# Performance work log

Measured on AMD Instinct MI355X. Metric: run time of the kernel, lower is better.

Reference implementation:

```python
import jax, jax.numpy as jnp
import numpy as np

EPS = 1e-12  # matches torch F.normalize default eps


def _l2_normalize(x, axis=-1):
    norm = jnp.sqrt(jnp.sum(x * x, axis=axis, keepdims=True))
    return x / jnp.maximum(norm, EPS)


def setup_inputs() -> dict:
    key = jax.random.key(0)
    k1, k2 = jax.random.split(key)
    B, D, P = 8192, 512, 32768
    z_context = jax.random.normal(k1, (B, D), dtype=jnp.float32)
    prototypes = jax.random.normal(k2, (P, D), dtype=jnp.float32) * 0.02
    return {"z_context": z_context, "prototypes": prototypes, "topk": 3}


def reference(z_context, prototypes, topk):
    # Cosine similarity: normalize queries and prototype bank, then GEMM.
    z_norm = _l2_normalize(z_context, axis=-1)          # [B, D]
    p_norm = _l2_normalize(prototypes, axis=-1)         # [P, D]
    sim = jnp.einsum('bd,pd->bp', z_norm, p_norm)       # [B, P]
    k = min(topk, prototypes.shape[0])
    topk_val, topk_idx = jax.lax.top_k(sim, k)          # [B, k] each
    return sim, topk_idx, topk_val
```

## Files before the change

### kernel.cpp

```cpp
#include <hip/hip_runtime.h>
#include <float.h>
#include <stdint.h>

#define D_DIM 512

typedef __attribute__((ext_vector_type(8))) short bf16x8;
typedef __attribute__((ext_vector_type(4))) float f32x4;

#define GLD_LDS16(g, l)                                              \
    __builtin_amdgcn_global_load_lds(                                \
        (const __attribute__((address_space(1))) void*)(g),          \
        (__attribute__((address_space(3))) void*)(l), 16, 0, 0)

__device__ __forceinline__ uint32_t pk_bf16(float a, float b) {
    uint32_t ua = __builtin_bit_cast(uint32_t, a) + 0x8000u;
    uint32_t ub = __builtin_bit_cast(uint32_t, b) + 0x8000u;
    return (ua >> 16) | (ub & 0xFFFF0000u);
}

__global__ __launch_bounds__(256) void convert_norm_kernel(
        const float* __restrict__ X, unsigned short* __restrict__ Xb,
        float* __restrict__ r, int R) {
    int row = blockIdx.x * 4 + (threadIdx.x >> 6);
    if (row >= R) return;
    int lane = threadIdx.x & 63;
    const float* x = X + (size_t)row * D_DIM + lane * 8;
    float4 f0 = *(const float4*)(x);
    float4 f1 = *(const float4*)(x + 4);
    float s = f0.x*f0.x + f0.y*f0.y + f0.z*f0.z + f0.w*f0.w
            + f1.x*f1.x + f1.y*f1.y + f1.z*f1.z + f1.w*f1.w;
#pragma unroll
    for (int off = 32; off; off >>= 1) s += __shfl_xor(s, off);
    float rv = 1.0f / fmaxf(sqrtf(s), 1e-12f);
    if (lane == 0) r[row] = rv;
    uint4 w;
    w.x = pk_bf16(f0.x * rv, f0.y * rv);
    w.y = pk_bf16(f0.z * rv, f0.w * rv);
    w.z = pk_bf16(f1.x * rv, f1.y * rv);
    w.w = pk_bf16(f1.z * rv, f1.w * rv);
    *(uint4*)(Xb + (size_t)row * D_DIM + lane * 8) = w;
}

template <bool FUSE>
__global__ __launch_bounds__(256, 4) void gemm_lds_bf16(
        const unsigned short* __restrict__ Zb,
        const unsigned short* __restrict__ Pb,
        float* __restrict__ sim, uint2* __restrict__ part, int Pn) {
    __shared__ __align__(16) unsigned char SH[32768];
    uint4* S = (uint4*)SH;

    int bi = blockIdx.x;
    int mb, nb;
    if (gridDim.x == 16384) {
        int xcd = bi & 7;
        int r = bi >> 3;
        mb = xcd * 8 + (r & 7);
        nb = r >> 3;
    } else {
        nb = bi % (Pn / 128);
        mb = bi / (Pn / 128);
    }
    const int bm = mb * 128, bn = nb * 128;

    const int tid = threadIdx.x;
    const int lane = tid & 63;
    const int wid = tid >> 6;
    const int wr = wid >> 1, wc = wid & 1;
    const int ln15 = lane & 15, hi = lane >> 4;

    const unsigned short* gA[2];
    const unsigned short* gB[2];
    int ldsIdx[2];
#pragma unroll
    for (int q = 0; q < 2; ++q) {
        int flat = q * 256 + tid;
        int row = flat >> 2;
        int c = flat & 3;
        int cg = c ^ (row & 3);
        gA[q] = Zb + (size_t)(bm + row) * D_DIM + cg * 8;
        gB[q] = Pb + (size_t)(bn + row) * D_DIM + cg * 8;
        ldsIdx[q] = flat;
    }

    f32x4 acc[4][4] = {};

#pragma unroll
    for (int q = 0; q < 2; ++q) {
        GLD_LDS16(gA[q], &S[ldsIdx[q]]);
        GLD_LDS16(gB[q], &S[512 + ldsIdx[q]]);
        gA[q] += 32;
        gB[q] += 32;
    }

    int cur = 0;
#pragma unroll 1
    for (int s8 = 0; s8 < 16; ++s8) {
        const int nxt = cur ^ 1;
        if (s8 < 15) {
#pragma unroll
            for (int q = 0; q < 2; ++q) {
                GLD_LDS16(gA[q], &S[nxt * 1024 + ldsIdx[q]]);
                GLD_LDS16(gB[q], &S[nxt * 1024 + 512 + ldsIdx[q]]);
                gA[q] += 32;
                gB[q] += 32;
            }
            asm volatile("s_waitcnt vmcnt(4)" ::: "memory");
        } else {
            asm volatile("s_waitcnt vmcnt(0)" ::: "memory");
        }
        __builtin_amdgcn_s_barrier();
        __builtin_amdgcn_sched_barrier(0);

        const int sb = cur * 1024;
        __builtin_amdgcn_s_setprio(1);
        bf16x8 av[4], bv[4];
#pragma unroll
        for (int t = 0; t < 4; ++t) {
            int arow = wr * 64 + t * 16 + ln15;
            av[t] = __builtin_bit_cast(bf16x8,
                    S[sb + arow * 4 + (hi ^ (arow & 3))]);
            int brow = wc * 64 + t * 16 + ln15;
            bv[t] = __builtin_bit_cast(bf16x8,
                    S[sb + 512 + brow * 4 + (hi ^ (brow & 3))]);
        }
#pragma unroll
        for (int i = 0; i < 4; ++i)
#pragma unroll
            for (int j = 0; j < 4; ++j)
                acc[i][j] = __builtin_amdgcn_mfma_f32_16x16x32_bf16(
                    av[i], bv[j], acc[i][j], 0, 0, 0);
        __builtin_amdgcn_s_setprio(0);
        __builtin_amdgcn_sched_barrier(0);
        __builtin_amdgcn_s_barrier();
        cur = nxt;
    }

#pragma unroll
    for (int i = 0; i < 4; ++i) {
#pragma unroll
        for (int rr = 0; rr < 4; ++rr) {
            int row = bm + wr * 64 + i * 16 + hi * 4 + rr;
#pragma unroll
            for (int j = 0; j < 4; ++j) {
                int col = bn + wc * 64 + j * 16 + ln15;
                sim[(size_t)row * Pn + col] = acc[i][j][rr];
            }
        }
    }

    if constexpr (FUSE) {
        float* T = (float*)SH;
        uint2* M = (uint2*)(SH + 17408);
        const int NB = Pn >> 7;
        const int r = tid & 63;
        const int q = tid >> 6;
#pragma unroll 1
        for (int hf = 0; hf < 2; ++hf) {
            float rv[4]; int ri[4];
#pragma unroll
            for (int k = 0; k < 4; ++k) { rv[k] = -FLT_MAX; ri[k] = 0x7FFFFFFF; }
#pragma unroll 1
            for (int ch = 0; ch < 2; ++ch) {
                __syncthreads();
                if (wr == hf && wc == ch) {
#pragma unroll
                    for (int i = 0; i < 4; ++i)
#pragma unroll
                        for (int j = 0; j < 4; ++j)
                            *(f32x4*)&T[(j * 16 + ln15) * 68 + i * 16 + hi * 4]
                                = acc[i][j];
                }
                __syncthreads();
                float tv[4]; int ti[4];
#pragma unroll
                for (int k = 0; k < 4; ++k) { tv[k] = -FLT_MAX; ti[k] = 0x7FFFFFFF; }
#pragma unroll
                for (int c4 = 0; c4 < 16; c4 += 4) {
                    float e0 = T[(q * 16 + c4 + 0) * 68 + r];
                    float e1 = T[(q * 16 + c4 + 1) * 68 + r];
                    float e2 = T[(q * 16 + c4 + 2) * 68 + r];
                    float e3 = T[(q * 16 + c4 + 3) * 68 + r];
                    float mg = fmaxf(fmaxf(e0, e1), fmaxf(e2, e3));
                    if (mg > tv[3]) {
                        float ee[4] = {e0, e1, e2, e3};
#pragma unroll
                        for (int e = 0; e < 4; ++e) {
                            float val = ee[e];
                            if (val > tv[3]) {
                                int p = 3;
#pragma unroll
                                for (int j2 = 2; j2 >= 0; --j2)
                                    if (val > tv[j2]) { tv[j2+1] = tv[j2]; ti[j2+1] = ti[j2]; p = j2; }
                                tv[p] = val; ti[p] = bn + ch * 64 + q * 16 + c4 + e;
                            }
                        }
                    }
                }
#pragma unroll
                for (int k = 0; k < 4; ++k)
                    M[q * 256 + k * 64 + r] =
                        make_uint2(__builtin_bit_cast(uint32_t, tv[k]), (uint32_t)ti[k]);
                __syncthreads();
                if (tid < 64) {
#pragma unroll
                    for (int qq = 0; qq < 4; ++qq)
#pragma unroll
                        for (int k = 0; k < 4; ++k) {
                            uint2 u = M[qq * 256 + k * 64 + tid];
                            float val = __builtin_bit_cast(float, u.x);
                            if (val > rv[3]) {
                                int p = 3;
#pragma unroll
                                for (int j2 = 2; j2 >= 0; --j2)
                                    if (val > rv[j2]) { rv[j2+1] = rv[j2]; ri[j2+1] = ri[j2]; p = j2; }
                                rv[p] = val; ri[p] = (int)u.y;
                            }
                        }
                }
            }
            if (tid < 64) {
                size_t o = ((size_t)(bm + hf * 64 + tid) * NB + nb) * 4;
#pragma unroll
                for (int k = 0; k < 4; ++k)
                    part[o + k] =
                        make_uint2(__builtin_bit_cast(uint32_t, rv[k]), (uint32_t)ri[k]);
            }
        }
    }
}

__global__ __launch_bounds__(256) void topk_reduce(const uint2* __restrict__ part,
        const float* __restrict__ Z, const float* __restrict__ Pm,
        const float* __restrict__ rz, const float* __restrict__ rp,
        float* __restrict__ oidx, float* __restrict__ oval, int Pn) {
    int row = blockIdx.x * 4 + (threadIdx.x >> 6);
    int lane = threadIdx.x & 63;
    const int NB = Pn >> 7;
    const uint2* pr = part + (size_t)row * NB * 4;

    float v[8]; int ix[8];
#pragma unroll
    for (int j = 0; j < 8; ++j) { v[j] = -FLT_MAX; ix[j] = -1; }

    const int total = NB * 4;
    for (int c = lane; c < total; c += 64) {
        uint2 u = pr[c];
        float val = __builtin_bit_cast(float, u.x);
        if (val > v[7]) {
            int idx = (int)u.y;
            int pos = 7;
#pragma unroll
            for (int j = 6; j >= 0; --j) {
                if (val > v[j]) { v[j+1] = v[j]; ix[j+1] = ix[j]; pos = j; }
            }
            v[pos] = val; ix[pos] = idx;
        }
    }

    int cand[8];
#pragma unroll
    for (int k = 0; k < 8; ++k) {
        float bv = v[0]; int bi2 = ix[0];
#pragma unroll
        for (int off = 32; off; off >>= 1) {
            float ov = __shfl_xor(bv, off);
            int oi = __shfl_xor(bi2, off);
            if (ov > bv || (ov == bv && oi >= 0 && (unsigned)oi < (unsigned)bi2)) {
                bv = ov; bi2 = oi;
            }
        }
        cand[k] = bi2;
        if (bi2 == ix[0]) {
#pragma unroll
            for (int j = 0; j < 7; ++j) { v[j] = v[j+1]; ix[j] = ix[j+1]; }
            v[7] = -FLT_MAX; ix[7] = -1;
        }
    }

    float zv[8];
    const float* zrow = Z + (size_t)row * D_DIM + lane * 8;
#pragma unroll
    for (int j = 0; j < 8; ++j) zv[j] = zrow[j];
    float rzv = rz[row];

    float ex[8];
#pragma unroll
    for (int c = 0; c < 8; ++c) {
        int idx = cand[c];
        const float* prow = Pm + (size_t)idx * D_DIM + lane * 8;
        float s = 0.f;
#pragma unroll
        for (int j = 0; j < 8; ++j) s += zv[j] * prow[j];
#pragma unroll
        for (int off = 32; off; off >>= 1) s += __shfl_xor(s, off);
        ex[c] = s * rzv * rp[idx];
    }

    bool used[8] = {};
#pragma unroll
    for (int k = 0; k < 3; ++k) {
        float bv = -FLT_MAX; int bi2 = Pn; int bc = 0;
#pragma unroll
        for (int c = 0; c < 8; ++c) {
            if (!used[c] && (ex[c] > bv || (ex[c] == bv && cand[c] < bi2))) {
                bv = ex[c]; bi2 = cand[c]; bc = c;
            }
        }
        used[bc] = true;
        if (lane == 0) {
            oidx[(size_t)row * 3 + k] = (float)bi2;
            oval[(size_t)row * 3 + k] = bv;
        }
    }
}

__global__ __launch_bounds__(256) void rnorm_kernel(const float* __restrict__ X,
                                                    float* __restrict__ r, int R) {
    int row = blockIdx.x * 4 + (threadIdx.x >> 6);
    if (row >= R) return;
    int lane = threadIdx.x & 63;
    const float* x = X + (size_t)row * D_DIM;
    float s = 0.f;
#pragma unroll
    for (int t = 0; t < 2; ++t) {
        float4 v = *(const float4*)(x + (t * 64 + lane) * 4);
        s += v.x * v.x + v.y * v.y + v.z * v.z + v.w * v.w;
    }
#pragma unroll
    for (int off = 32; off; off >>= 1) s += __shfl_xor(s, off);
    if (lane == 0) r[row] = 1.0f / fmaxf(sqrtf(s), 1e-12f);
}

__global__ __launch_bounds__(256, 2) void gemm_bf16_sim(const float* __restrict__ Z,
        const float* __restrict__ Pm, const float* __restrict__ rz,
        const float* __restrict__ rp, float* __restrict__ sim, int Pn) {
    __shared__ uint4 As16[1024];
    __shared__ uint4 Bs16[1024];
    int bi = blockIdx.x;
    int mb, nb;
    if (gridDim.x == 16384) {
        int xcd = bi & 7;
        int r = bi >> 3;
        mb = xcd * 8 + (r & 7);
        nb = r >> 3;
    } else {
        nb = bi % (Pn / 128);
        mb = bi / (Pn / 128);
    }
    const int bm = mb * 128, bn = nb * 128;
    const int tid = threadIdx.x;
    const int srow = tid >> 1;
    const int half = tid & 1;
    const float* aP = Z  + (size_t)(bm + srow) * D_DIM + half * 32;
    const float* bP = Pm + (size_t)(bn + srow) * D_DIM + half * 32;
    const int lane = tid & 63;
    const int wid = tid >> 6;
    const int wr = wid >> 1, wc = wid & 1;
    const int ln15 = lane & 15, hi = lane >> 4;
    f32x4 acc[4][4] = {};
    float4 f[8], g[8];
#pragma unroll
    for (int q = 0; q < 8; ++q) {
        f[q] = *(const float4*)(aP + q * 4);
        g[q] = *(const float4*)(bP + q * 4);
    }
#pragma unroll 1
    for (int s = 0; s < 8; ++s) {
#pragma unroll
        for (int q8 = 0; q8 < 4; ++q8) {
            uint4 wa, wb;
            wa.x = pk_bf16(f[2*q8].x,   f[2*q8].y);
            wa.y = pk_bf16(f[2*q8].z,   f[2*q8].w);
            wa.z = pk_bf16(f[2*q8+1].x, f[2*q8+1].y);
            wa.w = pk_bf16(f[2*q8+1].z, f[2*q8+1].w);
            wb.x = pk_bf16(g[2*q8].x,   g[2*q8].y);
            wb.y = pk_bf16(g[2*q8].z,   g[2*q8].w);
            wb.z = pk_bf16(g[2*q8+1].x, g[2*q8+1].y);
            wb.w = pk_bf16(g[2*q8+1].z, g[2*q8+1].w);
            int colByte = half * 64 + q8 * 16;
            int idx = srow * 8 + ((colByte ^ ((srow & 7) << 4)) >> 4);
            As16[idx] = wa;
            Bs16[idx] = wb;
        }
        __syncthreads();
        if (s < 7) {
            int k0 = (s + 1) * 64;
#pragma unroll
            for (int q = 0; q < 8; ++q) {
                f[q] = *(const float4*)(aP + k0 + q * 4);
                g[q] = *(const float4*)(bP + k0 + q * 4);
            }
        }
#pragma unroll
        for (int kk = 0; kk < 2; ++kk) {
            bf16x8 av[4], bv[4];
            const int cb = kk * 64 + hi * 16;
#pragma unroll
            for (int t = 0; t < 4; ++t) {
                int arow = wr * 64 + t * 16 + ln15;
                av[t] = __builtin_bit_cast(bf16x8,
                        As16[arow * 8 + ((cb ^ ((arow & 7) << 4)) >> 4)]);
                int brow = wc * 64 + t * 16 + ln15;
                bv[t] = __builtin_bit_cast(bf16x8,
                        Bs16[brow * 8 + ((cb ^ ((brow & 7) << 4)) >> 4)]);
            }
#pragma unroll
            for (int i = 0; i < 4; ++i)
#pragma unroll
                for (int j = 0; j < 4; ++j)
                    acc[i][j] = __builtin_amdgcn_mfma_f32_16x16x32_bf16(
                        av[i], bv[j], acc[i][j], 0, 0, 0);
        }
        __syncthreads();
    }
    float rpv[4];
#pragma unroll
    for (int j = 0; j < 4; ++j) rpv[j] = rp[bn + wc * 64 + j * 16 + ln15];
#pragma unroll
    for (int i = 0; i < 4; ++i) {
#pragma unroll
        for (int rr = 0; rr < 4; ++rr) {
            int row = bm + wr * 64 + i * 16 + hi * 4 + rr;
            float rzv = rz[row];
#pragma unroll
            for (int j = 0; j < 4; ++j) {
                int col = bn + wc * 64 + j * 16 + ln15;
                sim[(size_t)row * Pn + col] = acc[i][j][rr] * rzv * rpv[j];
            }
        }
    }
}

__global__ __launch_bounds__(256) void topk_refine(const float* __restrict__ sim,
        const float* __restrict__ Z, const float* __restrict__ Pm,
        const float* __restrict__ rz, const float* __restrict__ rp,
        float* __restrict__ oidx, float* __restrict__ oval, int Pn) {
    int row = blockIdx.x * 4 + (threadIdx.x >> 6);
    int lane = threadIdx.x & 63;
    const float* rptr = sim + (size_t)row * Pn;

    float v[8]; int ix[8];
#pragma unroll
    for (int j = 0; j < 8; ++j) { v[j] = -FLT_MAX; ix[j] = -1; }

    const int iters = Pn >> 8;
    for (int t = 0; t < iters; ++t) {
        int base = t * 256 + lane * 4;
        float4 q = *(const float4*)(rptr + base);
        float vals[4] = {q.x, q.y, q.z, q.w};
#pragma unroll
        for (int e = 0; e < 4; ++e) {
            float val = vals[e];
            if (val > v[7]) {
                int idx = base + e;
                int pos = 7;
#pragma unroll
                for (int j = 6; j >= 0; --j) {
                    if (val > v[j]) { v[j+1] = v[j]; ix[j+1] = ix[j]; pos = j; }
                }
                v[pos] = val; ix[pos] = idx;
            }
        }
    }

    int cand[8];
#pragma unroll
    for (int k = 0; k < 8; ++k) {
        float bv = v[0]; int bi2 = ix[0];
#pragma unroll
        for (int off = 32; off; off >>= 1) {
            float ov = __shfl_xor(bv, off);
            int oi = __shfl_xor(bi2, off);
            if (ov > bv || (ov == bv && oi >= 0 && (unsigned)oi < (unsigned)bi2)) {
                bv = ov; bi2 = oi;
            }
        }
        cand[k] = bi2;
        if (bi2 == ix[0]) {
#pragma unroll
            for (int j = 0; j < 7; ++j) { v[j] = v[j+1]; ix[j] = ix[j+1]; }
            v[7] = -FLT_MAX; ix[7] = -1;
        }
    }

    float zv[8];
    const float* zrow = Z + (size_t)row * D_DIM + lane * 8;
#pragma unroll
    for (int j = 0; j < 8; ++j) zv[j] = zrow[j];
    float rzv = rz[row];

    float ex[8];
#pragma unroll
    for (int c = 0; c < 8; ++c) {
        int idx = cand[c];
        const float* prow = Pm + (size_t)idx * D_DIM + lane * 8;
        float s = 0.f;
#pragma unroll
        for (int j = 0; j < 8; ++j) s += zv[j] * prow[j];
#pragma unroll
        for (int off = 32; off; off >>= 1) s += __shfl_xor(s, off);
        ex[c] = s * rzv * rp[idx];
    }

    bool used[8] = {};
#pragma unroll
    for (int k = 0; k < 3; ++k) {
        float bv = -FLT_MAX; int bi2 = Pn; int bc = 0;
#pragma unroll
        for (int c = 0; c < 8; ++c) {
            if (!used[c] && (ex[c] > bv || (ex[c] == bv && cand[c] < bi2))) {
                bv = ex[c]; bi2 = cand[c]; bc = c;
            }
        }
        used[bc] = true;
        if (lane == 0) {
            oidx[(size_t)row * 3 + k] = (float)bi2;
            oval[(size_t)row * 3 + k] = bv;
        }
    }
}

extern "C" void kernel_launch(void* const* d_in, const int* in_sizes, int n_in,
                              void* d_out, int out_size, void* d_ws, size_t ws_size,
                              hipStream_t stream) {
    const float* Z  = (const float*)d_in[0];
    const float* Pm = (const float*)d_in[1];
    const int B  = in_sizes[0] / D_DIM;
    const int Pn = in_sizes[1] / D_DIM;

    float* sim  = (float*)d_out;
    float* oidx = sim + (size_t)B * Pn;
    float* oval = oidx + (size_t)B * 3;

    float* rz = (float*)d_ws;
    float* rp = rz + B;
    unsigned short* Zb = (unsigned short*)(rp + Pn);
    unsigned short* Pb = Zb + (size_t)B * D_DIM;
    uint2* part = (uint2*)(Pb + (size_t)Pn * D_DIM);

    const size_t NB = (size_t)Pn / 128;
    const size_t need_bf16  = (size_t)(B + Pn) * 4 + (size_t)(B + Pn) * D_DIM * 2;
    const size_t need_fused = need_bf16 + (size_t)B * NB * 4 * sizeof(uint2);

    dim3 grid((B / 128) * (Pn / 128));

    if (ws_size >= need_fused) {
        convert_norm_kernel<<<B / 4, 256, 0, stream>>>(Z, Zb, rz, B);
        convert_norm_kernel<<<Pn / 4, 256, 0, stream>>>(Pm, Pb, rp, Pn);
        gemm_lds_bf16<true><<<grid, 256, 0, stream>>>(Zb, Pb, sim, part, Pn);
        topk_reduce<<<B / 4, 256, 0, stream>>>(part, Z, Pm, rz, rp, oidx, oval, Pn);
    } else if (ws_size >= need_bf16) {
        convert_norm_kernel<<<B / 4, 256, 0, stream>>>(Z, Zb, rz, B);
        convert_norm_kernel<<<Pn / 4, 256, 0, stream>>>(Pm, Pb, rp, Pn);
        gemm_lds_bf16<false><<<grid, 256, 0, stream>>>(Zb, Pb, sim, nullptr, Pn);
        topk_refine<<<B / 4, 256, 0, stream>>>(sim, Z, Pm, rz, rp, oidx, oval, Pn);
    } else {
        rnorm_kernel<<<B / 4, 256, 0, stream>>>(Z, rz, B);
        rnorm_kernel<<<Pn / 4, 256, 0, stream>>>(Pm, rp, Pn);
        gemm_bf16_sim<<<grid, 256, 0, stream>>>(Z, Pm, rz, rp, sim, Pn);
        topk_refine<<<B / 4, 256, 0, stream>>>(sim, Z, Pm, rz, rp, oidx, oval, Pn);
    }
}
```

Before: 695.6 us.

## Add 256x256-tile fused GEMM with coalesced sim stores and per-tile top-k

Adds a new 512-thread GEMM kernel that uses 256x256 output tiles with a 64-wide K step, double-buffered direct global-to-LDS loads and 128 KB of dynamic shared memory. It fuses the top-k partial selection and writes sim through an LDS transpose, so each thread stores full float4 rows. The larger tile halves redundant operand reads and halves the number of partial top-k entries the reduce kernel has to scan. In exchange it holds more accumulator registers per thread and needs a large LDS allocation, which may limit occupancy. The insertion sort is also rewritten as a macro.

```diff
diff --git a/kernel.cpp b/kernel.cpp
--- a/kernel.cpp
+++ b/kernel.cpp
@@ -17,6 +17,15 @@
     uint32_t ub = __builtin_bit_cast(uint32_t, b) + 0x8000u;
     return (ua >> 16) | (ub & 0xFFFF0000u);
 }
+
+#define INS4(val, idx, tv, ti)                                        \
+    if ((val) > tv[3]) {                                              \
+        int p_ = 3;                                                   \
+        if ((val) > tv[2]) { tv[3] = tv[2]; ti[3] = ti[2]; p_ = 2; }  \
+        if ((val) > tv[1]) { tv[2] = tv[1]; ti[2] = ti[1]; p_ = 1; }  \
+        if ((val) > tv[0]) { tv[1] = tv[0]; ti[1] = ti[0]; p_ = 0; }  \
+        tv[p_] = (val); ti[p_] = (idx);                               \
+    }
 
 __global__ __launch_bounds__(256) void convert_norm_kernel(
         const float* __restrict__ X, unsigned short* __restrict__ Xb,
@@ -41,13 +50,274 @@
     *(uint4*)(Xb + (size_t)row * D_DIM + lane * 8) = w;
 }
 
+__global__ __launch_bounds__(512, 2) void gemm256_fused(
+        const unsigned short* __restrict__ Zb,
+        const unsigned short* __restrict__ Pb,
+        float* __restrict__ sim, uint2* __restrict__ part, int Pn) {
+    extern __shared__ __align__(16) unsigned char SH[];
+    uint4* S = (uint4*)SH;
+
+    int bi = blockIdx.x;
+    int mb, nb;
+    if (gridDim.x == 4096) {
+        int xcd = bi & 7, r = bi >> 3;
+        mb = xcd * 4 + (r & 3);
+        nb = r >> 2;
+    } else {
+        int nt = Pn >> 8;
+        nb = bi % nt; mb = bi / nt;
+    }
+    const int bm = mb << 8, bn = nb << 8;
+
+    const int tid = threadIdx.x;
+    const int lane = tid & 63;
+    const int wid = tid >> 6;
+    const int wr = wid >> 2;
+    const int wc = wid & 3;
+    const int ln15 = lane & 15, hi = lane >> 4;
+
+    const int fl0 = tid, fl1 = 512 + tid;
+    const int rl0 = fl0 >> 3, rl1 = fl1 >> 3;
+    const int cg0 = (fl0 & 7) ^ (rl0 & 7);
+    const int cg1 = (fl1 & 7) ^ (rl1 & 7);
+
+    const unsigned short* pA0q0 = Zb + (size_t)(bm + rl0) * D_DIM + cg0 * 8;
+    const unsigned short* pA0q1 = Zb + (size_t)(bm + rl1) * D_DIM + cg1 * 8;
+    const unsigned short* pA1q0 = Zb + (size_t)(bm + 128 + rl0) * D_DIM + cg0 * 8;
+    const unsigned short* pA1q1 = Zb + (size_t)(bm + 128 + rl1) * D_DIM + cg1 * 8;
+    const unsigned short* pB0q0 = Pb + (size_t)(bn + rl0) * D_DIM + cg0 * 8;
+    const unsigned short* pB0q1 = Pb + (size_t)(bn + rl1) * D_DIM + cg1 * 8;
+    const unsigned short* pB1q0 = Pb + (size_t)(bn + 128 + rl0) * D_DIM + cg0 * 8;
+    const unsigned short* pB1q1 = Pb + (size_t)(bn + 128 + rl1) * D_DIM + cg1 * 8;
+
+    const int dA0q0 = fl0,        dA0q1 = fl1;
+    const int dA1q0 = 1024 + fl0, dA1q1 = 1024 + fl1;
+    const int dB0q0 = 4096 + fl0, dB0q1 = 4096 + fl1;
+    const int dB1q0 = 5120 + fl0, dB1q1 = 5120 + fl1;
+
+    const int sw0 = hi ^ (ln15 & 7);
+    const int sw1 = (4 + hi) ^ (ln15 & 7);
+    int aOff[8], bOff[4];
+#pragma unroll
+    for (int m = 0; m < 8; ++m) aOff[m] = (wr * 128 + m * 16 + ln15) * 8;
+#pragma unroll
+    for (int n = 0; n < 4; ++n) bOff[n] = 4096 + (wc * 64 + n * 16 + ln15) * 8;
+
+    f32x4 acc[8][4] = {};
+
+    GLD_LDS16(pA0q0, &S[dA0q0]); GLD_LDS16(pA0q1, &S[dA0q1]);
+    GLD_LDS16(pA1q0, &S[dA1q0]); GLD_LDS16(pA1q1, &S[dA1q1]);
+    GLD_LDS16(pB0q0, &S[dB0q0]); GLD_LDS16(pB0q1, &S[dB0q1]);
+    GLD_LDS16(pB1q0, &S[dB1q0]); GLD_LDS16(pB1q1, &S[dB1q1]);
+    pA0q0 += 64; pA0q1 += 64; pA1q0 += 64; pA1q1 += 64;
+    pB0q0 += 64; pB0q1 += 64; pB1q0 += 64; pB1q1 += 64;
+    asm volatile("s_waitcnt vmcnt(0)" ::: "memory");
+    __builtin_amdgcn_s_barrier();
+
+#pragma unroll 1
+    for (int t = 0; t < 8; ++t) {
+        const int db = (t & 1) * 2048;
+        const int dn = ((t + 1) & 1) * 2048;
+        const bool more = (t < 7);
+#pragma unroll
+        for (int p = 0; p < 4; ++p) {
+            const int mh = p >> 1, nh = p & 1;
+            bf16x8 av[4][2], bv[2][2];
+#pragma unroll
+            for (int mi = 0; mi < 4; ++mi) {
+                av[mi][0] = __builtin_bit_cast(bf16x8, S[db + aOff[mh * 4 + mi] + sw0]);
+                av[mi][1] = __builtin_bit_cast(bf16x8, S[db + aOff[mh * 4 + mi] + sw1]);
+            }
+#pragma unroll
+            for (int ni = 0; ni < 2; ++ni) {
+                bv[ni][0] = __builtin_bit_cast(bf16x8, S[db + bOff[nh * 2 + ni] + sw0]);
+                bv[ni][1] = __builtin_bit_cast(bf16x8, S[db + bOff[nh * 2 + ni] + sw1]);
+            }
+            if (p == 0 && more) {
+                GLD_LDS16(pB0q0, &S[dn + dB0q0]); GLD_LDS16(pB0q1, &S[dn + dB0q1]);
+                GLD_LDS16(pA0q0, &S[dn + dA0q0]); GLD_LDS16(pA0q1, &S[dn + dA0q1]);
+                pB0q0 += 64; pB0q1 += 64; pA0q0 += 64; pA0q1 += 64;
+            }
+            if (p == 1 && more) {
+                GLD_LDS16(pB1q0, &S[dn + dB1q0]); GLD_LDS16(pB1q1, &S[dn + dB1q1]);
+                GLD_LDS16(pA1q0, &S[dn + dA1q0]); GLD_LDS16(pA1q1, &S[dn + dA1q1]);
+                pB1q0 += 64; pB1q1 += 64; pA1q0 += 64; pA1q1 += 64;
+            }
+            __builtin_amdgcn_s_barrier();
+            asm volatile("s_waitcnt lgkmcnt(0)" ::: "memory");
+            __builtin_amdgcn_sched_barrier(0);
+            __builtin_amdgcn_s_setprio(1);
+#pragma unroll
+            for (int kk = 0; kk < 2; ++kk)
+#pragma unroll
+                for (int mi = 0; mi < 4; ++mi)
+#pragma unroll
+                    for (int ni = 0; ni < 2; ++ni)
+                        acc[mh * 4 + mi][nh * 2 + ni] =
+                            __builtin_amdgcn_mfma_f32_16x16x32_bf16(
+                                av[mi][kk], bv[ni][kk],
+                                acc[mh * 4 + mi][nh * 2 + ni], 0, 0, 0);
+            __builtin_amdgcn_s_setprio(0);
+            __builtin_amdgcn_sched_barrier(0);
+            if (p < 3) __builtin_amdgcn_s_barrier();
+        }
+        if (more) asm volatile("s_waitcnt vmcnt(0)" ::: "memory");
+        __builtin_amdgcn_s_barrier();
+    }
+
+    float* T = (float*)SH;
+    const int NB = Pn >> 8;
+    const int r = tid >> 2;
+    const int g = tid & 3;
+#pragma unroll 1
+    for (int hf = 0; hf < 2; ++hf) {
+        float tv[4]; int ti[4];
+#pragma unroll
+        for (int k = 0; k < 4; ++k) { tv[k] = -FLT_MAX; ti[k] = 0x7FFFFFFF; }
+#pragma unroll 1
+        for (int ch = 0; ch < 2; ++ch) {
+            __syncthreads();
+            if (wr == hf && (wc >> 1) == ch) {
+#pragma unroll
+                for (int m = 0; m < 8; ++m)
+#pragma unroll
+                    for (int n = 0; n < 4; ++n)
+                        *(f32x4*)&T[((wc & 1) * 64 + n * 16 + ln15) * 132
+                                    + m * 16 + hi * 4] = acc[m][n];
+            }
+            __syncthreads();
+            const int colBase = bn + ch * 128;
+            float* srow = sim + (size_t)(bm + hf * 128 + r) * Pn + colBase;
+#pragma unroll
+            for (int j = 0; j < 8; ++j) {
+                const int c0 = j * 16 + g * 4;
+                float e0 = T[(c0 + 0) * 132 + r];
+                float e1 = T[(c0 + 1) * 132 + r];
+                float e2 = T[(c0 + 2) * 132 + r];
+                float e3 = T[(c0 + 3) * 132 + r];
+                float4 o; o.x = e0; o.y = e1; o.z = e2; o.w = e3;
+                *(float4*)&srow[c0] = o;
+                float mg = fmaxf(fmaxf(e0, e1), fmaxf(e2, e3));
+                if (mg > tv[3]) {
+                    INS4(e0, colBase + c0 + 0, tv, ti);
+                    INS4(e1, colBase + c0 + 1, tv, ti);
+                    INS4(e2, colBase + c0 + 2, tv, ti);
+                    INS4(e3, colBase + c0 + 3, tv, ti);
+                }
+            }
+        }
+#pragma unroll
+        for (int st = 1; st <= 2; st <<= 1) {
+            float ov0 = __shfl_xor(tv[0], st), ov1 = __shfl_xor(tv[1], st);
+            float ov2 = __shfl_xor(tv[2], st), ov3 = __shfl_xor(tv[3], st);
+            int oi0 = __shfl_xor(ti[0], st), oi1 = __shfl_xor(ti[1], st);
+            int oi2 = __shfl_xor(ti[2], st), oi3 = __shfl_xor(ti[3], st);
+            INS4(ov0, oi0, tv, ti);
+            INS4(ov1, oi1, tv, ti);
+            INS4(ov2, oi2, tv, ti);
+            INS4(ov3, oi3, tv, ti);
+        }
+        if (g == 0) {
+            size_t o = ((size_t)(bm + hf * 128 + r) * NB + nb) * 4;
+#pragma unroll
+            for (int k = 0; k < 4; ++k)
+                part[o + k] =
+                    make_uint2(__builtin_bit_cast(uint32_t, tv[k]), (uint32_t)ti[k]);
+        }
+    }
+}
+
+__global__ __launch_bounds__(256) void topk_reduce(const uint2* __restrict__ part,
+        const float* __restrict__ Z, const float* __restrict__ Pm,
+        const float* __restrict__ rz, const float* __restrict__ rp,
+        float* __restrict__ oidx, float* __restrict__ oval, int Pn, int NB) {
+    int row = blockIdx.x * 4 + (threadIdx.x >> 6);
+    int lane = threadIdx.x & 63;
+    const uint2* pr = part + (size_t)row * NB * 4;
+
+    float v[8]; int ix[8];
+#pragma unroll
+    for (int j = 0; j < 8; ++j) { v[j] = -FLT_MAX; ix[j] = -1; }
+
+    const int total = NB * 4;
+    for (int c = lane; c < total; c += 64) {
+        uint2 u = pr[c];
+        float val = __builtin_bit_cast(float, u.x);
+        if (val > v[7]) {
+            int idx = (int)u.y;
+            int pos = 7;
+#pragma unroll
+            for (int j = 6; j >= 0; --j) {
+                if (val > v[j]) { v[j+1] = v[j]; ix[j+1] = ix[j]; pos = j; }
+            }
+            v[pos] = val; ix[pos] = idx;
+        }
+    }
+
+    int cand[8];
+#pragma unroll
+    for (int k = 0; k < 8; ++k) {
+        float bv = v[0]; int bi2 = ix[0];
+#pragma unroll
+        for (int off = 32; off; off >>= 1) {
+            float ov = __shfl_xor(bv, off);
+            int oi = __shfl_xor(bi2, off);
+            if (ov > bv || (ov == bv && oi >= 0 && (unsigned)oi < (unsigned)bi2)) {
+                bv = ov; bi2 = oi;
+            }
+        }
+        cand[k] = bi2;
+        if (bi2 == ix[0]) {
+#pragma unroll
+            for (int j = 0; j < 7; ++j) { v[j] = v[j+1]; ix[j] = ix[j+1]; }
+            v[7] = -FLT_MAX; ix[7] = -1;
+        }
+    }
+
+    float zv[8];
+    const float* zrow = Z + (size_t)row * D_DIM + lane * 8;
+#pragma unroll
+    for (int j = 0; j < 8; ++j) zv[j] = zrow[j];
+    float rzv = rz[row];
+
+    float ex[8];
+#pragma unroll
+    for (int c = 0; c < 8; ++c) {
+        int idx = cand[c];
+        const float* prow = Pm + (size_t)idx * D_DIM + lane * 8;
+        float s = 0.f;
+#pragma unroll
+        for (int j = 0; j < 8; ++j) s += zv[j] * prow[j];
+#pragma unroll
+        for (int off = 32; off; off >>= 1) s += __shfl_xor(s, off);
+        ex[c] = s * rzv * rp[idx];
+    }
+
+    bool used[8] = {};
+#pragma unroll
+    for (int k = 0; k < 3; ++k) {
+        float bv = -FLT_MAX; int bi2 = Pn; int bc = 0;
+#pragma unroll
+        for (int c = 0; c < 8; ++c) {
+            if (!used[c] && (ex[c] > bv || (ex[c] == bv && cand[c] < bi2))) {
+                bv = ex[c]; bi2 = cand[c]; bc = c;
+            }
+        }
+        used[bc] = true;
+        if (lane == 0) {
+            oidx[(size_t)row * 3 + k] = (float)bi2;
+            oval[(size_t)row * 3 + k] = bv;
+        }
+    }
+}
+
 template <bool FUSE>
 __global__ __launch_bounds__(256, 4) void gemm_lds_bf16(
         const unsigned short* __restrict__ Zb,
         const unsigned short* __restrict__ Pb,
         float* __restrict__ sim, uint2* __restrict__ part, int Pn) {
-    __shared__ __align__(16) unsigned char SH[32768];
-    uint4* S = (uint4*)SH;
+    __shared__ __align__(16) unsigned char SHs[32768];
+    uint4* S = (uint4*)SHs;
 
     int bi = blockIdx.x;
     int mb, nb;
@@ -149,8 +419,8 @@
     }
 
     if constexpr (FUSE) {
-        float* T = (float*)SH;
-        uint2* M = (uint2*)(SH + 17408);
+        float* T = (float*)SHs;
+        uint2* M = (uint2*)(SHs + 17408);
         const int NB = Pn >> 7;
         const int r = tid & 63;
         const int q = tid >> 6;
@@ -182,18 +452,11 @@
                     float e3 = T[(q * 16 + c4 + 3) * 68 + r];
                     float mg = fmaxf(fmaxf(e0, e1), fmaxf(e2, e3));
                     if (mg > tv[3]) {
-                        float ee[4] = {e0, e1, e2, e3};
-#pragma unroll
-                        for (int e = 0; e < 4; ++e) {
-                            float val = ee[e];
-                            if (val > tv[3]) {
-                                int p = 3;
-#pragma unroll
-                                for (int j2 = 2; j2 >= 0; --j2)
-                                    if (val > tv[j2]) { tv[j2+1] = tv[j2]; ti[j2+1] = ti[j2]; p = j2; }
-                                tv[p] = val; ti[p] = bn + ch * 64 + q * 16 + c4 + e;
-                            }
-                        }
+                        int cb = bn + ch * 64 + q * 16 + c4;
+                        INS4(e0, cb + 0, tv, ti);
+                        INS4(e1, cb + 1, tv, ti);
+                        INS4(e2, cb + 2, tv, ti);
+                        INS4(e3, cb + 3, tv, ti);
                     }
                 }
 #pragma unroll
@@ -208,13 +471,7 @@
                         for (int k = 0; k < 4; ++k) {
                             uint2 u = M[qq * 256 + k * 64 + tid];
                             float val = __builtin_bit_cast(float, u.x);
-                            if (val > rv[3]) {
-                                int p = 3;
-#pragma unroll
-                                for (int j2 = 2; j2 >= 0; --j2)
-                                    if (val > rv[j2]) { rv[j2+1] = rv[j2]; ri[j2+1] = ri[j2]; p = j2; }
-                                rv[p] = val; ri[p] = (int)u.y;
-                            }
+                            INS4(val, (int)u.y, rv, ri);
                         }
                 }
             }
@@ -225,91 +482,6 @@
                     part[o + k] =
                         make_uint2(__builtin_bit_cast(uint32_t, rv[k]), (uint32_t)ri[k]);
             }
-        }
-    }
-}
-
-__global__ __launch_bounds__(256) void topk_reduce(const uint2* __restrict__ part,
-        const float* __restrict__ Z, const float* __restrict__ Pm,
-        const float* __restrict__ rz, const float* __restrict__ rp,
-        float* __restrict__ oidx, float* __restrict__ oval, int Pn) {
-    int row = blockIdx.x * 4 + (threadIdx.x >> 6);
-    int lane = threadIdx.x & 63;
-    const int NB = Pn >> 7;
-    const uint2* pr = part + (size_t)row * NB * 4;
-
-    float v[8]; int ix[8];
-#pragma unroll
-    for (int j = 0; j < 8; ++j) { v[j] = -FLT_MAX; ix[j] = -1; }
-
-    const int total = NB * 4;
-    for (int c = lane; c < total; c += 64) {
-        uint2 u = pr[c];
-        float val = __builtin_bit_cast(float, u.x);
-        if (val > v[7]) {
-            int idx = (int)u.y;
-            int pos = 7;
-#pragma unroll
-            for (int j = 6; j >= 0; --j) {
-                if (val > v[j]) { v[j+1] = v[j]; ix[j+1] = ix[j]; pos = j; }
-            }
-            v[pos] = val; ix[pos] = idx;
-        }
-    }
-
-    int cand[8];
-#pragma unroll
-    for (int k = 0; k < 8; ++k) {
-        float bv = v[0]; int bi2 = ix[0];
-#pragma unroll
-        for (int off = 32; off; off >>= 1) {
-            float ov = __shfl_xor(bv, off);
-            int oi = __shfl_xor(bi2, off);
-            if (ov > bv || (ov == bv && oi >= 0 && (unsigned)oi < (unsigned)bi2)) {
-                bv = ov; bi2 = oi;
-            }
-        }
-        cand[k] = bi2;
-        if (bi2 == ix[0]) {
-#pragma unroll
-            for (int j = 0; j < 7; ++j) { v[j] = v[j+1]; ix[j] = ix[j+1]; }
-            v[7] = -FLT_MAX; ix[7] = -1;
-        }
-    }
-
-    float zv[8];
-    const float* zrow = Z + (size_t)row * D_DIM + lane * 8;
-#pragma unroll
-    for (int j = 0; j < 8; ++j) zv[j] = zrow[j];
-    float rzv = rz[row];
-
-    float ex[8];
-#pragma unroll
-    for (int c = 0; c < 8; ++c) {
-        int idx = cand[c];
-        const float* prow = Pm + (size_t)idx * D_DIM + lane * 8;
-        float s = 0.f;
-#pragma unroll
-        for (int j = 0; j < 8; ++j) s += zv[j] * prow[j];
-#pragma unroll
-        for (int off = 32; off; off >>= 1) s += __shfl_xor(s, off);
-        ex[c] = s * rzv * rp[idx];
-    }
-
-    bool used[8] = {};
-#pragma unroll
-    for (int k = 0; k < 3; ++k) {
-        float bv = -FLT_MAX; int bi2 = Pn; int bc = 0;
-#pragma unroll
-        for (int c = 0; c < 8; ++c) {
-            if (!used[c] && (ex[c] > bv || (ex[c] == bv && cand[c] < bi2))) {
-                bv = ex[c]; bi2 = cand[c]; bc = c;
-            }
-        }
-        used[bc] = true;
-        if (lane == 0) {
-            oidx[(size_t)row * 3 + k] = (float)bi2;
-            oval[(size_t)row * 3 + k] = bv;
         }
     }
 }
@@ -337,16 +509,8 @@
     __shared__ uint4 As16[1024];
     __shared__ uint4 Bs16[1024];
     int bi = blockIdx.x;
-    int mb, nb;
-    if (gridDim.x == 16384) {
-        int xcd = bi & 7;
-        int r = bi >> 3;
-        mb = xcd * 8 + (r & 7);
-        nb = r >> 3;
-    } else {
-        nb = bi % (Pn / 128);
-        mb = bi / (Pn / 128);
-    }
+    int nb = bi % (Pn / 128);
+    int mb = bi / (Pn / 128);
     const int bm = mb * 128, bn = nb * 128;
     const int tid = threadIdx.x;
     const int srow = tid >> 1;
@@ -538,26 +702,42 @@
     unsigned short* Pb = Zb + (size_t)B * D_DIM;
     uint2* part = (uint2*)(Pb + (size_t)Pn * D_DIM);
 
-    const size_t NB = (size_t)Pn / 128;
-    const size_t need_bf16  = (size_t)(B + Pn) * 4 + (size_t)(B + Pn) * D_DIM * 2;
-    const size_t need_fused = need_bf16 + (size_t)B * NB * 4 * sizeof(uint2);
-
-    dim3 grid((B / 128) * (Pn / 128));
-
-    if (ws_size >= need_fused) {
+    const size_t need_bf16 = (size_t)(B + Pn) * 4 + (size_t)(B + Pn) * D_DIM * 2;
+    const size_t need256 = need_bf16 + (size_t)B * (Pn >> 8) * 4 * sizeof(uint2);
+    const size_t need128 = need_bf16 + (size_t)B * (Pn >> 7) * 4 * sizeof(uint2);
+
+    bool big = false;
+    if ((B & 255) == 0 && (Pn & 255) == 0 && ws_size >= need256) {
+        big = (hipFuncSetAttribute((const void*)gemm256_fused,
+                   hipFuncAttributeMaxDynamicSharedMemorySize,
+                   131072) == hipSuccess);
+    }
+
+    if (big) {
         convert_norm_kernel<<<B / 4, 256, 0, stream>>>(Z, Zb, rz, B);
         convert_norm_kernel<<<Pn / 4, 256, 0, stream>>>(Pm, Pb, rp, Pn);
-        gemm_lds_bf16<true><<<grid, 256, 0, stream>>>(Zb, Pb, sim, part, Pn);
-        topk_reduce<<<B / 4, 256, 0, stream>>>(part, Z, Pm, rz, rp, oidx, oval, Pn);
+        gemm256_fused<<<(B / 256) * (Pn / 256), 512, 131072, stream>>>(
+            Zb, Pb, sim, part, Pn);
+        topk_reduce<<<B / 4, 256, 0, stream>>>(part, Z, Pm, rz, rp,
+                                               oidx, oval, Pn, Pn >> 8);
+    } else if (ws_size >= need128) {
+        convert_norm_kernel<<<B / 4, 256, 0, stream>>>(Z, Zb, rz, B);
+        convert_norm_kernel<<<Pn / 4, 256, 0, stream>>>(Pm, Pb, rp, Pn);
+        gemm_lds_bf16<true><<<(B / 128) * (Pn / 128), 256, 0, stream>>>(
+            Zb, Pb, sim, part, Pn);
+        topk_reduce<<<B / 4, 256, 0, stream>>>(part, Z, Pm, rz, rp,
+                                               oidx, oval, Pn, Pn >> 7);
     } else if (ws_size >= need_bf16) {
         convert_norm_kernel<<<B / 4, 256, 0, stream>>>(Z, Zb, rz, B);
         convert_norm_kernel<<<Pn / 4, 256, 0, stream>>>(Pm, Pb, rp, Pn);
-        gemm_lds_bf16<false><<<grid, 256, 0, stream>>>(Zb, Pb, sim, nullptr, Pn);
+        gemm_lds_bf16<false><<<(B / 128) * (Pn / 128), 256, 0, stream>>>(
+            Zb, Pb, sim, nullptr, Pn);
         topk_refine<<<B / 4, 256, 0, stream>>>(sim, Z, Pm, rz, rp, oidx, oval, Pn);
     } else {
         rnorm_kernel<<<B / 4, 256, 0, stream>>>(Z, rz, B);
         rnorm_kernel<<<Pn / 4, 256, 0, stream>>>(Pm, rp, Pn);
-        gemm_bf16_sim<<<grid, 256, 0, stream>>>(Z, Pm, rz, rp, sim, Pn);
+        gemm_bf16_sim<<<(B / 128) * (Pn / 128), 256, 0, stream>>>(
+            Z, Pm, rz, rp, sim, Pn);
         topk_refine<<<B / 4, 256, 0, stream>>>(sim, Z, Pm, rz, rp, oidx, oval, Pn);
     }
 }
```

Result: no change. 699.3 us (+0.5%).
